# Kernel tuning notes

Measured on AMD Instinct MI355X. Metric: run time of the kernel, lower is better.

Reference implementation:

```python
import jax, jax.numpy as jnp
import numpy as np
from jax import lax

NEG = -1e30


def ctc_loss(log_probs, targets, input_lengths, target_lengths, blank=0):
    """CTC loss per sample (reduction='none').
    log_probs: [B,T,C] log-softmaxed. targets: [B,S] int (values != blank).
    Returns [B] negative log likelihoods.
    """
    B, T, C = log_probs.shape
    S = targets.shape[1]
    L = 2 * S + 1
    # extended label sequence with blanks interleaved: [b, t1, b, t2, ..., b]
    blanks = jnp.full((B, S), blank, targets.dtype)
    ext = jnp.concatenate(
        [jnp.stack([blanks, targets], axis=-1).reshape(B, 2 * S),
         jnp.full((B, 1), blank, targets.dtype)], axis=1)  # [B,L]
    # skip-transition allowed where ext[l] != blank and ext[l] != ext[l-2]
    prev2 = jnp.concatenate([jnp.full((B, 2), -1, ext.dtype), ext[:, :-2]], axis=1)
    allow_skip = (ext != blank) & (ext != prev2)  # [B,L]

    lp0 = jnp.take_along_axis(log_probs[:, 0, :], ext, axis=1)  # [B,L]
    alpha0 = jnp.where(jnp.arange(L)[None, :] < 2, lp0, NEG)

    def step(alpha, lp_t):  # lp_t: [B,C]
        lp = jnp.take_along_axis(lp_t, ext, axis=1)  # [B,L]
        a1 = alpha
        a2 = jnp.concatenate([jnp.full((B, 1), NEG), alpha[:, :-1]], axis=1)
        a3 = jnp.where(allow_skip,
                       jnp.concatenate([jnp.full((B, 2), NEG), alpha[:, :-2]], axis=1),
                       NEG)
        new = jax.nn.logsumexp(jnp.stack([a1, a2, a3]), axis=0) + lp
        return new, new

    _, alphas = lax.scan(step, alpha0, jnp.swapaxes(log_probs, 0, 1)[1:])
    alphas = jnp.concatenate([alpha0[None], alphas], axis=0)  # [T,B,L]

    t_idx = jnp.clip(input_lengths - 1, 0, T - 1)
    alpha_T = alphas[t_idx, jnp.arange(B)]  # [B,L]
    l1 = jnp.clip(2 * target_lengths, 0, L - 1)
    l2 = jnp.clip(2 * target_lengths - 1, 0, L - 1)
    last = jnp.take_along_axis(alpha_T, jnp.stack([l1, l2], axis=1), axis=1)  # [B,2]
    return -jax.nn.logsumexp(last, axis=1)


def focal_ctc(logits, targets, input_lengths, target_lengths, alpha=1.0, gamma=2.0):
    log_probs = jax.nn.log_softmax(logits, axis=-1)
    l = jnp.clip(ctc_loss(log_probs, targets, input_lengths, target_lengths), 1e-6, None)
    p_t = jnp.clip(jnp.exp(-l), 1e-6, 1.0)
    return jnp.mean(alpha * (1.0 - p_t) ** gamma * l)


def setup_inputs() -> dict:
    key = jax.random.key(0)
    ks = jax.random.split(key, 8)
    B, T = 32, 2000
    C_err, C_ph = 8, 128
    S_err, S_ph = 50, 200
    return {
        "error_logits": jax.random.normal(ks[0], (B, T, C_err), jnp.float32),
        "phoneme_logits": jax.random.normal(ks[1], (B, T, C_ph), jnp.float32),
        "error_targets": jax.random.randint(ks[2], (B, S_err), 1, C_err, jnp.int32),
        "phoneme_targets": jax.random.randint(ks[3], (B, S_ph), 1, C_ph, jnp.int32),
        "error_input_lengths": jnp.full((B,), T, jnp.int32),
        "phoneme_input_lengths": jnp.full((B,), T, jnp.int32),
        "error_target_lengths": jax.random.randint(ks[4], (B,), S_err // 2, S_err + 1, jnp.int32),
        "phoneme_target_lengths": jax.random.randint(ks[5], (B,), S_ph // 2, S_ph + 1, jnp.int32),
    }


def reference(error_logits, phoneme_logits, error_targets, phoneme_targets,
              error_input_lengths, phoneme_input_lengths,
              error_target_lengths, phoneme_target_lengths):
    error_weight, phoneme_weight = 1.0, 1.0
    err = focal_ctc(error_logits, error_targets, error_input_lengths, error_target_lengths)
    ph = focal_ctc(phoneme_logits, phoneme_targets, phoneme_input_lengths, phoneme_target_lengths)
    total = error_weight * err + phoneme_weight * ph
    return total, err, ph
```

## Files before the change

kernel.cpp:

```cpp
#include <hip/hip_runtime.h>
#include <hip/hip_bf16.h>

#define LOG2E 1.4426950408889634f
#define LN2   0.6931471805599453f
#define NEG2  (-1.4426950e30f)
#define EXP2F(x) __builtin_exp2f(x)
#define LOG2F(x) __builtin_log2f(x)
#define LDEXPF(x,k) __builtin_ldexpf((x),(k))

__device__ __forceinline__ float dpp_shr1_f(float x, float old) {
    return __int_as_float(__builtin_amdgcn_update_dpp(
        __float_as_int(old), __float_as_int(x), 0x138, 0xF, 0xF, false));
}
__device__ __forceinline__ int dpp_shr1_i(int x, int old) {
    return __builtin_amdgcn_update_dpp(old, x, 0x138, 0xF, 0xF, false);
}
__device__ __forceinline__ float dpp_shl1_f(float x, float old) {
    return __int_as_float(__builtin_amdgcn_update_dpp(
        __float_as_int(old), __float_as_int(x), 0x130, 0xF, 0xF, false));
}
__device__ __forceinline__ int dpp_shl1_i(int x, int old) {
    return __builtin_amdgcn_update_dpp(old, x, 0x130, 0xF, 0xF, false);
}

__device__ __forceinline__ unsigned bf16r(float x) {
    return (__float_as_uint(x) + 0x8000u) >> 16;
}

__device__ __forceinline__ void async16(void* lds, const void* g) {
    __builtin_amdgcn_global_load_lds(
        (const __attribute__((address_space(1))) unsigned int*)g,
        (__attribute__((address_space(3))) unsigned int*)lds, 16, 0, 0);
}
__device__ __forceinline__ void async4(void* lds, const void* g) {
    __builtin_amdgcn_global_load_lds(
        (const __attribute__((address_space(1))) unsigned int*)g,
        (__attribute__((address_space(3))) unsigned int*)lds, 4, 0, 0);
}

__device__ __forceinline__ void unpack8(const uint4& q, float (&p)[8]) {
    p[0] = __uint_as_float(q.x << 16);
    p[1] = __uint_as_float(q.x & 0xFFFF0000u);
    p[2] = __uint_as_float(q.y << 16);
    p[3] = __uint_as_float(q.y & 0xFFFF0000u);
    p[4] = __uint_as_float(q.z << 16);
    p[5] = __uint_as_float(q.z & 0xFFFF0000u);
    p[6] = __uint_as_float(q.w << 16);
    p[7] = __uint_as_float(q.w & 0xFFFF0000u);
}

__global__ __launch_bounds__(256) void ph_prob_kernel(
    const float* __restrict__ logits, const int* __restrict__ tgt,
    unsigned short* __restrict__ P) {
    int wid = threadIdx.x >> 6, lane = threadIdx.x & 63;
    int r = blockIdx.x * 4 + wid;
    int b = r / 2000;
    const float* row = logits + (size_t)r * 128;
    __shared__ float ylds[4][128];
    float y0 = row[lane] * LOG2E;
    float y1 = row[lane + 64] * LOG2E;
    ylds[wid][lane] = y0;
    ylds[wid][lane + 64] = y1;
    float m = fmaxf(y0, y1);
#pragma unroll
    for (int i = 1; i < 64; i <<= 1) m = fmaxf(m, __shfl_xor(m, i));
    float s = EXP2F(y0 - m) + EXP2F(y1 - m);
#pragma unroll
    for (int i = 1; i < 64; i <<= 1) s += __shfl_xor(s, i);
    float d2 = m + LOG2F(s);

    int c[4];
#pragma unroll
    for (int k = 0; k < 4; ++k) {
        int i = min(4 * lane + k, 199);
        c[k] = tgt[b * 200 + i];
    }
    float pb = EXP2F(ylds[wid][0] - d2);
    float po[4];
#pragma unroll
    for (int k = 0; k < 4; ++k) po[k] = EXP2F(ylds[wid][c[k]] - d2);

    unsigned h[8];
#pragma unroll
    for (int s2 = 0; s2 < 8; ++s2) {
        int l = 8 * lane + s2;
        float v = (s2 & 1) ? po[s2 >> 1] : pb;
        h[s2] = (l <= 400) ? bf16r(v) : 0u;
    }
    uint4 u;
    u.x = h[0] | (h[1] << 16);
    u.y = h[2] | (h[3] << 16);
    u.z = h[4] | (h[5] << 16);
    u.w = h[6] | (h[7] << 16);
    *(uint4*)(P + (size_t)r * 512 + lane * 8) = u;
}

__global__ __launch_bounds__(256) void err_prob_kernel(
    const float* __restrict__ logits, const int* __restrict__ tgt,
    unsigned short* __restrict__ P) {
    int wid = threadIdx.x >> 6, lane = threadIdx.x & 63;
    int r = blockIdx.x * 4 + wid;
    int b = r / 2000;
    const float* row = logits + (size_t)r * 8;
    __shared__ float ylds[4][8];
    float y = (lane < 8) ? row[lane] * LOG2E : -3.0e38f;
    if (lane < 8) ylds[wid][lane] = y;
    float m = y;
#pragma unroll
    for (int i = 1; i < 64; i <<= 1) m = fmaxf(m, __shfl_xor(m, i));
    float s = EXP2F(y - m);
#pragma unroll
    for (int i = 1; i < 64; i <<= 1) s += __shfl_xor(s, i);
    float d2 = m + LOG2F(s);

    int cc = tgt[b * 50 + min(lane, 49)];
    float pb = EXP2F(ylds[wid][0] - d2);
    float pod = EXP2F(ylds[wid][cc] - d2);
    int l0 = 2 * lane;
    unsigned h0 = (l0 <= 100) ? bf16r(pb) : 0u;
    unsigned h1 = (l0 + 1 <= 100) ? bf16r(pod) : 0u;
    *(unsigned*)(P + (size_t)r * 128 + lane * 2) = h0 | (h1 << 16);
}

__device__ __forceinline__ void finish_loss(float capA, float capB, int capEA,
                                            int capEB, int lane,
                                            float* __restrict__ loss_out, int b) {
    float vA = (capA > 0.f) ? (float)capEA + LOG2F(capA) : NEG2;
    float vB = (capB > 0.f) ? (float)capEB + LOG2F(capB) : NEG2;
    float mm = fmaxf(vA, vB);
#pragma unroll
    for (int i = 1; i < 64; i <<= 1) mm = fmaxf(mm, __shfl_xor(mm, i));
    float sum = EXP2F(vA - mm) + EXP2F(vB - mm);
#pragma unroll
    for (int i = 1; i < 64; i <<= 1) sum += __shfl_xor(sum, i);
    if (lane == 0) loss_out[b] = -(mm + LOG2F(sum)) * LN2;
}

__global__ __launch_bounds__(64) void ctc6_kernel(
    const unsigned short* __restrict__ Perr, const unsigned short* __restrict__ Pph,
    const int* __restrict__ err_tgt, const int* __restrict__ ph_tgt,
    const int* __restrict__ err_il, const int* __restrict__ ph_il,
    const int* __restrict__ err_tl, const int* __restrict__ ph_tl,
    float* __restrict__ aerr, int* __restrict__ aerrE,
    float* __restrict__ gerr, int* __restrict__ gerrE,
    float* __restrict__ aph, int* __restrict__ aphE,
    float* __restrict__ gph, int* __restrict__ gphE,
    float* __restrict__ loss_err, float* __restrict__ loss_ph, int T) {
    __shared__ unsigned short ring[32 * 512];
    char* ringc = (char*)ring;
    const int blk = blockIdx.x;
    const int lane = threadIdx.x & 63;
    const int NR = T >> 1;
    const int NCH = NR >> 3;

    if (blk < 32) {
        const int b = blk;
        int t_idx = min(max(err_il[b] - 1, 0), T - 1);
        const int* tgt = err_tgt + b * 50;
        float skip1f;
        {
            int l = lane * 2 + 1; bool sk = false;
            if (l >= 3 && l <= 100) { int i = l >> 1; sk = (tgt[i] != tgt[i - 1]); }
            skip1f = sk ? 1.f : 0.f;
        }
        const char* base = (const char*)(Perr + (size_t)b * T * 128);
        float a0 = 0.f, a1 = 0.f; int E = 0;

        auto fstep = [&](unsigned cur, bool rn) {
            float p0 = __uint_as_float(cur << 16);
            float p1 = __uint_as_float(cur & 0xFFFF0000u);
            float n1 = dpp_shr1_f(a1, 0.f);
            int En = dpp_shr1_i(E, E);
            int Ep = max(E, En);
            float t1 = LDEXPF(n1, En - Ep);
            float o0 = LDEXPF(a0, E - Ep), o1 = LDEXPF(a1, E - Ep);
            E = Ep;
            a0 = (o0 + t1) * p0;
            a1 = __builtin_fmaf(skip1f, t1, o1 + o0) * p1;
            if (rn) {
                float m = fmaxf(a0, a1);
                int k = ((__float_as_int(m) >> 23) & 255) - 127;
                a0 = LDEXPF(a0, -k); a1 = LDEXPF(a1, -k); E += k;
            }
        };

        if (t_idx == T - 1) {
            const char* srcl = base + lane * 4;
            auto rd = [&](int row) -> unsigned {
                return *((const unsigned*)(ringc + (size_t)(row & 31) * 256) + lane);
            };
#pragma unroll
            for (int r = 0; r < 24; ++r)
                async4(ringc + (size_t)(r & 31) * 256, srcl + (size_t)r * 256);
            {
#pragma unroll
                for (int r = 24; r < 32; ++r)
                    async4(ringc + (size_t)(r & 31) * 256, srcl + (size_t)r * 256);
                asm volatile("s_waitcnt vmcnt(16)" ::: "memory");
                __builtin_amdgcn_sched_barrier(0);
                unsigned q[8];
#pragma unroll
                for (int j = 0; j < 8; ++j) q[j] = rd(j);
                float p0 = __uint_as_float(q[0] << 16);
                float p1 = __uint_as_float(q[0] & 0xFFFF0000u);
                a0 = (lane == 0) ? p0 : 0.f;
                a1 = (lane == 0) ? p1 : 0.f;
                E = 0;
#pragma unroll
                for (int j = 1; j < 8; ++j) fstep(q[j], (j == 3) || (j == 7));
            }
            for (int k = 1; k < NCH; ++k) {
                if (k + 3 < NCH) {
                    int bs = (k + 3) * 8;
#pragma unroll
                    for (int r = 0; r < 8; ++r)
                        async4(ringc + (size_t)((bs + r) & 31) * 256,
                               srcl + (size_t)(bs + r) * 256);
                    asm volatile("s_waitcnt vmcnt(16)" ::: "memory");
                } else {
                    asm volatile("s_waitcnt vmcnt(0)" ::: "memory");
                }
                __builtin_amdgcn_sched_barrier(0);
                unsigned q[8];
#pragma unroll
                for (int j = 0; j < 8; ++j) q[j] = rd(k * 8 + j);
#pragma unroll
                for (int j = 0; j < 8; ++j) fstep(q[j], (j == 3) || (j == 7));
            }
            aerr[b * 128 + lane * 2] = a0;
            aerr[b * 128 + lane * 2 + 1] = a1;
            aerrE[b * 64 + lane] = E;
        } else {
            const int L = 101; int tl = err_tl[b];
            int l1 = min(2 * tl, L - 1), l2 = max(min(2 * tl - 1, L - 1), 0);
            float capA = 0.f, capB = 0.f; int capEA = 0, capEB = 0;
            for (int t = 0; t < T; ++t) {
                unsigned cur = *((const unsigned*)(base + (size_t)t * 256) + lane);
                if (t == 0) {
                    float p0 = __uint_as_float(cur << 16);
                    float p1 = __uint_as_float(cur & 0xFFFF0000u);
                    a0 = (lane == 0) ? p0 : 0.f;
                    a1 = (lane == 0) ? p1 : 0.f;
                    E = 0;
                } else {
                    fstep(cur, false);
                }
                if (t == t_idx) {
                    int l0 = lane * 2;
                    if (l0 == l1) { capA = a0; capEA = E; }
                    if (l0 == l2) { capB = a0; capEB = E; }
                    if (l0 + 1 == l1) { capA = a1; capEA = E; }
                    if (l0 + 1 == l2) { capB = a1; capEB = E; }
                }
                if ((t & 3) == 3) {
                    float m = fmaxf(a0, a1);
                    int k = ((__float_as_int(m) >> 23) & 255) - 127;
                    a0 = LDEXPF(a0, -k); a1 = LDEXPF(a1, -k); E += k;
                }
            }
            finish_loss(capA, capB, capEA, capEB, lane, loss_err, b);
        }

    } else if (blk < 64) {
        const int b = blk - 32;
        const int* tgt = err_tgt + b * 50;
        const int L = 101; int tl = err_tl[b];
        int l1 = min(2 * tl, L - 1), l2 = max(min(2 * tl - 1, L - 1), 0);
        float skip1f;
        {
            int l = lane * 2 + 1; bool sk = false;
            if (l >= 3 && l <= 100) { int i = l >> 1; sk = (tgt[i] != tgt[i - 1]); }
            skip1f = sk ? 1.f : 0.f;
        }
        float skp2 = dpp_shl1_f(skip1f, 0.f);
        const char* base = (const char*)(Perr + (size_t)b * T * 128);
        const char* srcl = base + (size_t)(T - 1) * 256 + lane * 4;
        auto rd = [&](int row) -> unsigned {
            return *((const unsigned*)(ringc + (size_t)(row & 31) * 256) + lane);
        };
        float g0 = 0.f, g1 = 0.f; int E = 0;
        auto bstep = [&](unsigned cur, bool rn) {
            float p0 = __uint_as_float(cur << 16);
            float p1 = __uint_as_float(cur & 0xFFFF0000u);
            float nb0 = dpp_shl1_f(g0, 0.f), nb1 = dpp_shl1_f(g1, 0.f);
            int En = dpp_shl1_i(E, E);
            int Ep = max(E, En);
            float o0 = LDEXPF(g0, E - Ep), o1 = LDEXPF(g1, E - Ep);
            float t0 = LDEXPF(nb0, En - Ep), t1 = LDEXPF(nb1, En - Ep);
            E = Ep;
            g0 = (o0 + o1) * p0;
            g1 = __builtin_fmaf(skp2, t1, o1 + t0) * p1;
            if (rn) {
                float m = fmaxf(g0, g1);
                int k = ((__float_as_int(m) >> 23) & 255) - 127;
                g0 = LDEXPF(g0, -k); g1 = LDEXPF(g1, -k); E += k;
            }
        };
#pragma unroll
        for (int r = 0; r < 24; ++r)
            async4(ringc + (size_t)(r & 31) * 256, srcl - (size_t)r * 256);
        {
#pragma unroll
            for (int r = 24; r < 32; ++r)
                async4(ringc + (size_t)(r & 31) * 256, srcl - (size_t)r * 256);
            asm volatile("s_waitcnt vmcnt(16)" ::: "memory");
            __builtin_amdgcn_sched_barrier(0);
            unsigned q[8];
#pragma unroll
            for (int j = 0; j < 8; ++j) q[j] = rd(j);
            float p0 = __uint_as_float(q[0] << 16);
            float p1 = __uint_as_float(q[0] & 0xFFFF0000u);
            int l0 = lane * 2;
            g0 = (l0 == l1 || l0 == l2) ? p0 : 0.f;
            g1 = (l0 + 1 == l1 || l0 + 1 == l2) ? p1 : 0.f;
            E = 0;
#pragma unroll
            for (int j = 1; j < 8; ++j) bstep(q[j], (j == 3) || (j == 7));
        }
        for (int k = 1; k < NCH; ++k) {
            if (k + 3 < NCH) {
                int bs = (k + 3) * 8;
#pragma unroll
                for (int r = 0; r < 8; ++r)
                    async4(ringc + (size_t)((bs + r) & 31) * 256,
                           srcl - (size_t)(bs + r) * 256);
                asm volatile("s_waitcnt vmcnt(16)" ::: "memory");
            } else {
                asm volatile("s_waitcnt vmcnt(0)" ::: "memory");
            }
            __builtin_amdgcn_sched_barrier(0);
            unsigned q[8];
#pragma unroll
            for (int j = 0; j < 8; ++j) q[j] = rd(k * 8 + j);
#pragma unroll
            for (int j = 0; j < 8; ++j) bstep(q[j], (j == 3) || (j == 7));
        }
        gerr[b * 128 + lane * 2] = g0;
        gerr[b * 128 + lane * 2 + 1] = g1;
        gerrE[b * 64 + lane] = E;

    } else if (blk < 96) {
        const int b = blk - 64;
        int t_idx = min(max(ph_il[b] - 1, 0), T - 1);
        const int* tgt = ph_tgt + b * 200;
        float skf[8];
#pragma unroll
        for (int s = 0; s < 8; ++s) {
            int l = lane * 8 + s; float v = 0.f;
            if ((s & 1) && l >= 3 && l <= 400) {
                int i = l >> 1; v = (tgt[i] != tgt[i - 1]) ? 1.f : 0.f;
            }
            skf[s] = v;
        }
        const char* base = (const char*)(Pph + (size_t)b * T * 512);
        float a[8];
#pragma unroll
        for (int s = 0; s < 8; ++s) a[s] = 0.f;
        int E = 0;
        auto rd4 = [&](int row) -> uint4 {
            return *((const uint4*)(ringc + (size_t)(row & 31) * 1024) + lane);
        };
        auto fstep = [&](const uint4& q, bool rn) {
            float p[8]; unpack8(q, p);
            float n7 = dpp_shr1_f(a[7], 0.f), n6 = dpp_shr1_f(a[6], 0.f);
            int En = dpp_shr1_i(E, E);
            int Ep = max(E, En);
            float o[8];
#pragma unroll
            for (int s = 0; s < 8; ++s) o[s] = LDEXPF(a[s], E - Ep);
            float s7 = LDEXPF(n7, En - Ep), s6 = LDEXPF(n6, En - Ep);
            E = Ep;
#pragma unroll
            for (int s = 0; s < 8; ++s) {
                float am1 = (s == 0) ? s7 : o[s - 1];
                float am2 = (s == 0) ? s6 : ((s == 1) ? s7 : o[s - 2]);
                a[s] = __builtin_fmaf(skf[s], am2, o[s] + am1) * p[s];
            }
            if (rn) {
                float m = a[0];
#pragma unroll
                for (int s = 1; s < 8; ++s) m = fmaxf(m, a[s]);
                int k = ((__float_as_int(m) >> 23) & 255) - 127;
#pragma unroll
                for (int s = 0; s < 8; ++s) a[s] = LDEXPF(a[s], -k);
                E += k;
            }
        };

        if (t_idx == T - 1) {
            const char* srcl = base + lane * 16;
#pragma unroll
            for (int r = 0; r < 24; ++r)
                async16(ringc + (size_t)(r & 31) * 1024, srcl + (size_t)r * 1024);
            {
#pragma unroll
                for (int r = 24; r < 32; ++r)
                    async16(ringc + (size_t)(r & 31) * 1024, srcl + (size_t)r * 1024);
                asm volatile("s_waitcnt vmcnt(16)" ::: "memory");
                __builtin_amdgcn_sched_barrier(0);
                uint4 q[8];
#pragma unroll
                for (int j = 0; j < 8; ++j) q[j] = rd4(j);
                float p[8]; unpack8(q[0], p);
#pragma unroll
                for (int s = 0; s < 8; ++s) {
                    int l = lane * 8 + s;
                    a[s] = (l < 2) ? p[s] : 0.f;
                }
                E = 0;
#pragma unroll
                for (int j = 1; j < 8; ++j) fstep(q[j], (j == 3) || (j == 7));
            }
            for (int k = 1; k < NCH; ++k) {
                if (k + 3 < NCH) {
                    int bs = (k + 3) * 8;
#pragma unroll
                    for (int r = 0; r < 8; ++r)
                        async16(ringc + (size_t)((bs + r) & 31) * 1024,
                                srcl + (size_t)(bs + r) * 1024);
                    asm volatile("s_waitcnt vmcnt(16)" ::: "memory");
                } else {
                    asm volatile("s_waitcnt vmcnt(0)" ::: "memory");
                }
                __builtin_amdgcn_sched_barrier(0);
                uint4 q[8];
#pragma unroll
                for (int j = 0; j < 8; ++j) q[j] = rd4(k * 8 + j);
#pragma unroll
                for (int j = 0; j < 8; ++j) fstep(q[j], (j == 3) || (j == 7));
            }
#pragma unroll
            for (int s = 0; s < 8; ++s) aph[b * 512 + lane * 8 + s] = a[s];
            aphE[b * 64 + lane] = E;
        } else {
            const int L = 401; int tl = ph_tl[b];
            int l1 = min(2 * tl, L - 1), l2 = max(min(2 * tl - 1, L - 1), 0);
            float capA = 0.f, capB = 0.f; int capEA = 0, capEB = 0;
            for (int t = 0; t < T; ++t) {
                uint4 q = *((const uint4*)(base + (size_t)t * 1024) + lane);
                if (t == 0) {
                    float p[8]; unpack8(q, p);
#pragma unroll
                    for (int s = 0; s < 8; ++s) {
                        int l = lane * 8 + s;
                        a[s] = (l < 2) ? p[s] : 0.f;
                    }
                    E = 0;
                } else {
                    fstep(q, false);
                }
                if (t == t_idx) {
#pragma unroll
                    for (int s = 0; s < 8; ++s) {
                        int l = lane * 8 + s;
                        if (l == l1) { capA = a[s]; capEA = E; }
                        if (l == l2) { capB = a[s]; capEB = E; }
                    }
                }
                if ((t & 3) == 3) {
                    float m = a[0];
#pragma unroll
                    for (int s = 1; s < 8; ++s) m = fmaxf(m, a[s]);
                    int k = ((__float_as_int(m) >> 23) & 255) - 127;
#pragma unroll
                    for (int s = 0; s < 8; ++s) a[s] = LDEXPF(a[s], -k);
                    E += k;
                }
            }
            finish_loss(capA, capB, capEA, capEB, lane, loss_ph, b);
        }

    } else {
        const int b = blk - 96;
        const int* tgt = ph_tgt + b * 200;
        const int L = 401; int tl = ph_tl[b];
        int l1 = min(2 * tl, L - 1), l2 = max(min(2 * tl - 1, L - 1), 0);
        float skf[8];
#pragma unroll
        for (int s = 0; s < 8; ++s) {
            int l = lane * 8 + s; float v = 0.f;
            if ((s & 1) && l >= 3 && l <= 400) {
                int i = l >> 1; v = (tgt[i] != tgt[i - 1]) ? 1.f : 0.f;
            }
            skf[s] = v;
        }
        float nskf1 = dpp_shl1_f(skf[1], 0.f);
        float skp2[8];
        skp2[0] = 0.f; skp2[1] = skf[3]; skp2[2] = 0.f; skp2[3] = skf[5];
        skp2[4] = 0.f; skp2[5] = skf[7]; skp2[6] = 0.f; skp2[7] = nskf1;

        const char* base = (const char*)(Pph + (size_t)b * T * 512);
        const char* srcl = base + (size_t)(T - 1) * 1024 + lane * 16;
        auto rd4 = [&](int row) -> uint4 {
            return *((const uint4*)(ringc + (size_t)(row & 31) * 1024) + lane);
        };
        float g[8];
#pragma unroll
        for (int s = 0; s < 8; ++s) g[s] = 0.f;
        int E = 0;
        auto bstep = [&](const uint4& q, bool rn) {
            float p[8]; unpack8(q, p);
            float nb0 = dpp_shl1_f(g[0], 0.f), nb1 = dpp_shl1_f(g[1], 0.f);
            int En = dpp_shl1_i(E, E);
            int Ep = max(E, En);
            float o[8];
#pragma unroll
            for (int s = 0; s < 8; ++s) o[s] = LDEXPF(g[s], E - Ep);
            float t0 = LDEXPF(nb0, En - Ep), t1 = LDEXPF(nb1, En - Ep);
            E = Ep;
#pragma unroll
            for (int s = 0; s < 8; ++s) {
                float bp1 = (s < 7) ? o[s + 1] : t0;
                float bp2 = (s < 6) ? o[s + 2] : ((s == 6) ? t0 : t1);
                g[s] = __builtin_fmaf(skp2[s], bp2, o[s] + bp1) * p[s];
            }
            if (rn) {
                float m = g[0];
#pragma unroll
                for (int s = 1; s < 8; ++s) m = fmaxf(m, g[s]);
                int k = ((__float_as_int(m) >> 23) & 255) - 127;
#pragma unroll
                for (int s = 0; s < 8; ++s) g[s] = LDEXPF(g[s], -k);
                E += k;
            }
        };
#pragma unroll
        for (int r = 0; r < 24; ++r)
            async16(ringc + (size_t)(r & 31) * 1024, srcl - (size_t)r * 1024);
        {
#pragma unroll
            for (int r = 24; r < 32; ++r)
                async16(ringc + (size_t)(r & 31) * 1024, srcl - (size_t)r * 1024);
            asm volatile("s_waitcnt vmcnt(16)" ::: "memory");
            __builtin_amdgcn_sched_barrier(0);
            uint4 q[8];
#pragma unroll
            for (int j = 0; j < 8; ++j) q[j] = rd4(j);
            float p[8]; unpack8(q[0], p);
#pragma unroll
            for (int s = 0; s < 8; ++s) {
                int l = lane * 8 + s;
                g[s] = (l == l1 || l == l2) ? p[s] : 0.f;
            }
            E = 0;
#pragma unroll
            for (int j = 1; j < 8; ++j) bstep(q[j], (j == 3) || (j == 7));
        }
        for (int k = 1; k < NCH; ++k) {
            if (k + 3 < NCH) {
                int bs = (k + 3) * 8;
#pragma unroll
                for (int r = 0; r < 8; ++r)
                    async16(ringc + (size_t)((bs + r) & 31) * 1024,
                            srcl - (size_t)(bs + r) * 1024);
                asm volatile("s_waitcnt vmcnt(16)" ::: "memory");
            } else {
                asm volatile("s_waitcnt vmcnt(0)" ::: "memory");
            }
            __builtin_amdgcn_sched_barrier(0);
            uint4 q[8];
#pragma unroll
            for (int j = 0; j < 8; ++j) q[j] = rd4(k * 8 + j);
#pragma unroll
            for (int j = 0; j < 8; ++j) bstep(q[j], (j == 3) || (j == 7));
        }
#pragma unroll
        for (int s = 0; s < 8; ++s) gph[b * 512 + lane * 8 + s] = g[s];
        gphE[b * 64 + lane] = E;
    }
}

__global__ __launch_bounds__(64) void combine_kernel(
    const int* __restrict__ err_tgt, const int* __restrict__ ph_tgt,
    const int* __restrict__ err_il, const int* __restrict__ ph_il,
    const float* __restrict__ aerr, const int* __restrict__ aerrE,
    const float* __restrict__ gerr, const int* __restrict__ gerrE,
    const float* __restrict__ aph, const int* __restrict__ aphE,
    const float* __restrict__ gph, const int* __restrict__ gphE,
    float* __restrict__ loss_err, float* __restrict__ loss_ph, int T) {
    const int blk = blockIdx.x;
    const int lane = threadIdx.x & 63;
    if (blk < 32) {
        const int b = blk;
        int t_idx = min(max(err_il[b] - 1, 0), T - 1);
        if (t_idx != T - 1) return;
        const int* tgt = err_tgt + b * 50;
        float skip1f;
        {
            int l = lane * 2 + 1; bool sk = false;
            if (l >= 3 && l <= 100) { int i = l >> 1; sk = (tgt[i] != tgt[i - 1]); }
            skip1f = sk ? 1.f : 0.f;
        }
        float a0 = aerr[b * 128 + lane * 2], a1 = aerr[b * 128 + lane * 2 + 1];
        int Ea = aerrE[b * 64 + lane];
        float g0 = gerr[b * 128 + lane * 2], g1 = gerr[b * 128 + lane * 2 + 1];
        int Eb = gerrE[b * 64 + lane];
        float nb0 = __shfl_down(g0, 1), nb1 = __shfl_down(g1, 1);
        int Ebn = __shfl_down(Eb, 1);
        float skp2 = __shfl_down(skip1f, 1);
        if (lane == 63) { nb0 = 0.f; nb1 = 0.f; Ebn = Eb; skp2 = 0.f; }
        int Em = max(Eb, Ebn);
        float o0 = LDEXPF(g0, Eb - Em), o1 = LDEXPF(g1, Eb - Em);
        float t0 = LDEXPF(nb0, Ebn - Em), t1 = LDEXPF(nb1, Ebn - Em);
        float bc0 = o0 + o1;
        float bc1 = __builtin_fmaf(skp2, t1, o1 + t0);
        float dot = __builtin_fmaf(a0, bc0, a1 * bc1);
        float v = (dot > 0.f) ? (float)(Ea + Em) + LOG2F(dot) : NEG2;
        float mm = v;
#pragma unroll
        for (int i = 1; i < 64; i <<= 1) mm = fmaxf(mm, __shfl_xor(mm, i));
        float sum = EXP2F(v - mm);
#pragma unroll
        for (int i = 1; i < 64; i <<= 1) sum += __shfl_xor(sum, i);
        if (lane == 0) loss_err[b] = -(mm + LOG2F(sum)) * LN2;
    } else {
        const int b = blk - 32;
        int t_idx = min(max(ph_il[b] - 1, 0), T - 1);
        if (t_idx != T - 1) return;
        const int* tgt = ph_tgt + b * 200;
        float skf[8];
#pragma unroll
        for (int s = 0; s < 8; ++s) {
            int l = lane * 8 + s; float v = 0.f;
            if ((s & 1) && l >= 3 && l <= 400) {
                int i = l >> 1; v = (tgt[i] != tgt[i - 1]) ? 1.f : 0.f;
            }
            skf[s] = v;
        }
        float a[8], g[8];
#pragma unroll
        for (int s = 0; s < 8; ++s) {
            a[s] = aph[b * 512 + lane * 8 + s];
            g[s] = gph[b * 512 + lane * 8 + s];
        }
        int Ea = aphE[b * 64 + lane];
        int Eb = gphE[b * 64 + lane];
        float nb0 = __shfl_down(g[0], 1), nb1 = __shfl_down(g[1], 1);
        int Ebn = __shfl_down(Eb, 1);
        float nskf1 = __shfl_down(skf[1], 1);
        if (lane == 63) { nb0 = 0.f; nb1 = 0.f; Ebn = Eb; nskf1 = 0.f; }
        float skp2[8];
        skp2[0] = 0.f; skp2[1] = skf[3]; skp2[2] = 0.f; skp2[3] = skf[5];
        skp2[4] = 0.f; skp2[5] = skf[7]; skp2[6] = 0.f; skp2[7] = nskf1;
        int Em = max(Eb, Ebn);
        float o[8];
#pragma unroll
        for (int s = 0; s < 8; ++s) o[s] = LDEXPF(g[s], Eb - Em);
        float t0 = LDEXPF(nb0, Ebn - Em), t1 = LDEXPF(nb1, Ebn - Em);
        float dot = 0.f;
#pragma unroll
        for (int s = 0; s < 8; ++s) {
            float bp1 = (s < 7) ? o[s + 1] : t0;
            float bp2 = (s < 6) ? o[s + 2] : ((s == 6) ? t0 : t1);
            float bc = __builtin_fmaf(skp2[s], bp2, o[s] + bp1);
            dot = __builtin_fmaf(a[s], bc, dot);
        }
        float v = (dot > 0.f) ? (float)(Ea + Em) + LOG2F(dot) : NEG2;
        float mm = v;
#pragma unroll
        for (int i = 1; i < 64; i <<= 1) mm = fmaxf(mm, __shfl_xor(mm, i));
        float sum = EXP2F(v - mm);
#pragma unroll
        for (int i = 1; i < 64; i <<= 1) sum += __shfl_xor(sum, i);
        if (lane == 0) loss_ph[b] = -(mm + LOG2F(sum)) * LN2;
    }
}

__global__ void denom_err_kernel(const float* __restrict__ logits,
                                 float* __restrict__ d2, int rows) {
    int r = blockIdx.x * blockDim.x + threadIdx.x;
    if (r >= rows) return;
    const float* row = logits + (size_t)r * 8;
    float x[8];
#pragma unroll
    for (int i = 0; i < 8; ++i) x[i] = row[i] * LOG2E;
    float m = x[0];
#pragma unroll
    for (int i = 1; i < 8; ++i) m = fmaxf(m, x[i]);
    float s = 0.f;
#pragma unroll
    for (int i = 0; i < 8; ++i) s += EXP2F(x[i] - m);
    d2[r] = m + LOG2F(s);
}

__global__ void denom_ph_kernel(const float* __restrict__ logits,
                                float* __restrict__ d2, int rows) {
    int wave = (int)((blockIdx.x * (size_t)blockDim.x + threadIdx.x) >> 6);
    int lane = threadIdx.x & 63;
    if (wave >= rows) return;
    const float* row = logits + (size_t)wave * 128;
    float x0 = row[lane] * LOG2E;
    float x1 = row[lane + 64] * LOG2E;
    float m = fmaxf(x0, x1);
#pragma unroll
    for (int i = 1; i < 64; i <<= 1) m = fmaxf(m, __shfl_xor(m, i));
    float s = EXP2F(x0 - m) + EXP2F(x1 - m);
#pragma unroll
    for (int i = 1; i < 64; i <<= 1) s += __shfl_xor(s, i);
    if (lane == 0) d2[wave] = m + LOG2F(s);
}

template <int NST, int C>
__device__ __forceinline__ void gather_row(const float* ringL, const float* ringD,
                                           int row, const int (&clsoff)[NST],
                                           float (&g)[NST], float& gd) {
    int base = (row & 63) * C;
#pragma unroll
    for (int s = 0; s < NST; ++s) g[s] = ringL[base + clsoff[s]];
    gd = ringD[row & 63];
}

template <int C, int CHV>
__device__ __forceinline__ void stage_load(const float* __restrict__ lrow,
                                           const float* __restrict__ d2row,
                                           int t0, int T, int lane,
                                           float4 (&st)[CHV], float4& stD) {
#pragma unroll
// ... 93 lines not shown
        int li = v ? l : 0;
        int c = 0;
        bool sk = false;
        if (li & 1) {
            int i = li >> 1;
            c = tgt[i];
            if (li >= 3) sk = (c != tgt[i - 1]);
        }
        clsoff[s] = c;
        skipb[s] = sk;
        validf[s] = v ? 1.f : 0.f;
    }
    float4 st[CHV];
    float4 stD = make_float4(0.f, 0.f, 0.f, 0.f);
    stage_load<C, CHV>(lrow, d2row, 0, T, lane, st, stD);
    stage_write<C, CHV>(ringL, ringD, 0, lane, st, stD);
    stage_load<C, CHV>(lrow, d2row, 32, T, lane, st, stD);
    stage_write<C, CHV>(ringL, ringD, 32, lane, st, stD);
    stage_load<C, CHV>(lrow, d2row, 64, T, lane, st, stD);
    float gA[NST], gB[NST], dA, dB;
    gather_row<NST, C>(ringL, ringD, 0, clsoff, gA, dA);
    gather_row<NST, C>(ringL, ringD, 1, clsoff, gB, dB);
    float a[NST];
#pragma unroll
    for (int s = 0; s < NST; ++s) a[s] = 0.f;
    int E = 0;
    float capA = 0.f, capB = 0.f;
    int capEA = 0, capEB = 0;
    const int NCH = (T + 31) >> 5;
    for (int c = 0; c < NCH; ++c) {
        int t0 = c << 5;
        int half = min(32, T - t0) >> 1;
        for (int j = 0; j < half; ++j) {
            int t = t0 + 2 * j;
            do_step_lin<NST>(a, E, gA, dA, validf, skipb, lane, t, t_idx, l1, l2,
                             capA, capB, capEA, capEB);
            gather_row<NST, C>(ringL, ringD, t + 2, clsoff, gA, dA);
            do_step_lin<NST>(a, E, gB, dB, validf, skipb, lane, t + 1, t_idx, l1, l2,
                             capA, capB, capEA, capEB);
            gather_row<NST, C>(ringL, ringD, t + 3, clsoff, gB, dB);
            if (j == 14 && c + 2 < NCH) {
                stage_write<C, CHV>(ringL, ringD, t0 + 64, lane, st, stD);
                if (c + 3 < NCH)
                    stage_load<C, CHV>(lrow, d2row, t0 + 96, T, lane, st, stD);
            }
        }
    }
    float vA = (capA > 0.f) ? (float)capEA + LOG2F(capA) : NEG2;
    float vB = (capB > 0.f) ? (float)capEB + LOG2F(capB) : NEG2;
    float mm = fmaxf(vA, vB);
#pragma unroll
    for (int i = 1; i < 64; i <<= 1) mm = fmaxf(mm, __shfl_xor(mm, i));
    float sum = EXP2F(vA - mm) + EXP2F(vB - mm);
#pragma unroll
    for (int i = 1; i < 64; i <<= 1) sum += __shfl_xor(sum, i);
    if (lane == 0) loss_out[b] = -(mm + LOG2F(sum)) * LN2;
}

__global__ __launch_bounds__(64) void ctc_kernel(
    const float* __restrict__ err_logits, const float* __restrict__ ph_logits,
    const int* __restrict__ err_tgt, const int* __restrict__ ph_tgt,
    const int* __restrict__ err_il, const int* __restrict__ ph_il,
    const int* __restrict__ err_tl, const int* __restrict__ ph_tl,
    const float* __restrict__ d2_err, const float* __restrict__ d2_ph,
    float* __restrict__ loss_err, float* __restrict__ loss_ph, int T) {
    __shared__ float ringL[64 * 128];
    __shared__ float ringD[64];
    int blk = blockIdx.x;
    if (blk < 32) {
        int b = blk;
        const int L = 101;
        int tl = err_tl[b];
        int l1 = min(2 * tl, L - 1);
        int l2 = max(min(2 * tl - 1, L - 1), 0);
        int t_idx = min(max(err_il[b] - 1, 0), T - 1);
        ctc_run<2, 8, 50, 1>(err_logits + (size_t)b * T * 8, d2_err + (size_t)b * T,
                             err_tgt + b * 50, T, t_idx, l1, l2, ringL, ringD,
                             loss_err, b);
    } else {
        int b = blk - 32;
        const int L = 401;
        int tl = ph_tl[b];
        int l1 = min(2 * tl, L - 1);
        int l2 = max(min(2 * tl - 1, L - 1), 0);
        int t_idx = min(max(ph_il[b] - 1, 0), T - 1);
        ctc_run<8, 128, 200, 16>(ph_logits + (size_t)b * T * 128, d2_ph + (size_t)b * T,
                                 ph_tgt + b * 200, T, t_idx, l1, l2, ringL, ringD,
                                 loss_ph, b);
    }
}

__global__ void final_kernel(const float* __restrict__ loss_err,
                             const float* __restrict__ loss_ph,
                             float* __restrict__ out) {
    int lane = threadIdx.x & 63;
    float fe = 0.f, fp = 0.f;
    if (lane < 32) {
        float l = fmaxf(loss_err[lane], 1e-6f);
        float pt = fminf(fmaxf(EXP2F(-l * LOG2E), 1e-6f), 1.0f);
        float om = 1.f - pt;
        fe = om * om * l;
        l = fmaxf(loss_ph[lane], 1e-6f);
        pt = fminf(fmaxf(EXP2F(-l * LOG2E), 1e-6f), 1.0f);
        om = 1.f - pt;
        fp = om * om * l;
    }
#pragma unroll
    for (int i = 1; i < 64; i <<= 1) {
        fe += __shfl_xor(fe, i);
        fp += __shfl_xor(fp, i);
    }
    if (lane == 0) {
        float err = fe / 32.f;
        float ph = fp / 32.f;
        out[0] = err + ph;
        out[1] = err;
        out[2] = ph;
    }
}

extern "C" void kernel_launch(void* const* d_in, const int* in_sizes, int n_in,
                              void* d_out, int out_size, void* d_ws, size_t ws_size,
                              hipStream_t stream) {
    const int B = 32, T = 2000;
    const float* err_logits = (const float*)d_in[0];
    const float* ph_logits  = (const float*)d_in[1];
    const int* err_tgt = (const int*)d_in[2];
    const int* ph_tgt  = (const int*)d_in[3];
    const int* err_il  = (const int*)d_in[4];
    const int* ph_il   = (const int*)d_in[5];
    const int* err_tl  = (const int*)d_in[6];
    const int* ph_tl   = (const int*)d_in[7];
    float* out = (float*)d_out;

    const size_t PH_US  = (size_t)B * T * 512;
    const size_t ERR_US = (size_t)B * T * 128;

    char* p = (char*)d_ws;
    unsigned short* Pph  = (unsigned short*)p; p += PH_US * 2;
    unsigned short* Perr = (unsigned short*)p; p += ERR_US * 2;
    float* aph  = (float*)p; p += (size_t)B * 512 * 4;
    int*   aphE = (int*)p;   p += (size_t)B * 64 * 4;
    float* gph  = (float*)p; p += (size_t)B * 512 * 4;
    int*   gphE = (int*)p;   p += (size_t)B * 64 * 4;
    float* aerr = (float*)p; p += (size_t)B * 128 * 4;
    int*   aerrE= (int*)p;   p += (size_t)B * 64 * 4;
    float* gerr = (float*)p; p += (size_t)B * 128 * 4;
    int*   gerrE= (int*)p;   p += (size_t)B * 64 * 4;
    float* loss_err = (float*)p; p += B * 4;
    float* loss_ph  = (float*)p; p += B * 4;
    const size_t need = (size_t)(p - (char*)d_ws);

    if (ws_size >= need) {
        ph_prob_kernel<<<(B * T) / 4, 256, 0, stream>>>(ph_logits, ph_tgt, Pph);
        err_prob_kernel<<<(B * T) / 4, 256, 0, stream>>>(err_logits, err_tgt, Perr);
        ctc6_kernel<<<128, 64, 0, stream>>>(Perr, Pph, err_tgt, ph_tgt,
                                            err_il, ph_il, err_tl, ph_tl,
                                            aerr, aerrE, gerr, gerrE,
                                            aph, aphE, gph, gphE,
                                            loss_err, loss_ph, T);
        combine_kernel<<<64, 64, 0, stream>>>(err_tgt, ph_tgt, err_il, ph_il,
                                              aerr, aerrE, gerr, gerrE,
                                              aph, aphE, gph, gphE,
                                              loss_err, loss_ph, T);
        final_kernel<<<1, 64, 0, stream>>>(loss_err, loss_ph, out);
    } else {
        float* ws = (float*)d_ws;
        float* d2_err   = ws;
        float* d2_ph    = ws + 64000;
        float* le = ws + 128000;
        float* lp = ws + 128032;
        int rows = B * T;
        denom_err_kernel<<<(rows + 255) / 256, 256, 0, stream>>>(err_logits, d2_err, rows);
        denom_ph_kernel<<<rows / 4, 256, 0, stream>>>(ph_logits, d2_ph, rows);
        ctc_kernel<<<64, 64, 0, stream>>>(err_logits, ph_logits, err_tgt, ph_tgt,
                                          err_il, ph_il, err_tl, ph_tl,
                                          d2_err, d2_ph, le, lp, T);
        final_kernel<<<1, 64, 0, stream>>>(le, lp, out);
    }
}
```

Before: 184.4 us.

## Fuse prob kernels and hoist neighbor exponent alignment out of per-step recursion

Merges the phoneme and error probability kernels into one launch, with the grid split by block index. In the CTC forward and backward recursions, the per-timestep exponent alignment between neighbouring lanes (a DPP shift of E plus several ldexp calls) is moved into the periodic renormalization. A cached power-of-two scale factor f is applied to the shifted neighbour values at each step instead. This shortens the serial per-timestep dependency chain, at the cost of the neighbour's relative scale going stale for up to four steps. The d>=-127 clamp and the four-step growth between renormalizations could affect precision in edge cases.

```diff
diff --git a/kernel.cpp b/kernel.cpp
--- a/kernel.cpp
+++ b/kernel.cpp
@@ -49,77 +49,75 @@
     p[7] = __uint_as_float(q.w & 0xFFFF0000u);
 }
 
-__global__ __launch_bounds__(256) void ph_prob_kernel(
-    const float* __restrict__ logits, const int* __restrict__ tgt,
-    unsigned short* __restrict__ P) {
+__global__ __launch_bounds__(256) void prob_kernel(
+    const float* __restrict__ ph_logits, const int* __restrict__ ph_tgt,
+    unsigned short* __restrict__ Pph,
+    const float* __restrict__ err_logits, const int* __restrict__ err_tgt,
+    unsigned short* __restrict__ Perr) {
     int wid = threadIdx.x >> 6, lane = threadIdx.x & 63;
-    int r = blockIdx.x * 4 + wid;
-    int b = r / 2000;
-    const float* row = logits + (size_t)r * 128;
     __shared__ float ylds[4][128];
-    float y0 = row[lane] * LOG2E;
-    float y1 = row[lane + 64] * LOG2E;
-    ylds[wid][lane] = y0;
-    ylds[wid][lane + 64] = y1;
-    float m = fmaxf(y0, y1);
-#pragma unroll
-    for (int i = 1; i < 64; i <<= 1) m = fmaxf(m, __shfl_xor(m, i));
-    float s = EXP2F(y0 - m) + EXP2F(y1 - m);
-#pragma unroll
-    for (int i = 1; i < 64; i <<= 1) s += __shfl_xor(s, i);
-    float d2 = m + LOG2F(s);
-
-    int c[4];
-#pragma unroll
-    for (int k = 0; k < 4; ++k) {
-        int i = min(4 * lane + k, 199);
-        c[k] = tgt[b * 200 + i];
-    }
-    float pb = EXP2F(ylds[wid][0] - d2);
-    float po[4];
-#pragma unroll
-    for (int k = 0; k < 4; ++k) po[k] = EXP2F(ylds[wid][c[k]] - d2);
-
-    unsigned h[8];
-#pragma unroll
-    for (int s2 = 0; s2 < 8; ++s2) {
-        int l = 8 * lane + s2;
-        float v = (s2 & 1) ? po[s2 >> 1] : pb;
-        h[s2] = (l <= 400) ? bf16r(v) : 0u;
-    }
-    uint4 u;
-    u.x = h[0] | (h[1] << 16);
-    u.y = h[2] | (h[3] << 16);
-    u.z = h[4] | (h[5] << 16);
-    u.w = h[6] | (h[7] << 16);
-    *(uint4*)(P + (size_t)r * 512 + lane * 8) = u;
-}
-
-__global__ __launch_bounds__(256) void err_prob_kernel(
-    const float* __restrict__ logits, const int* __restrict__ tgt,
-    unsigned short* __restrict__ P) {
-    int wid = threadIdx.x >> 6, lane = threadIdx.x & 63;
-    int r = blockIdx.x * 4 + wid;
-    int b = r / 2000;
-    const float* row = logits + (size_t)r * 8;
-    __shared__ float ylds[4][8];
-    float y = (lane < 8) ? row[lane] * LOG2E : -3.0e38f;
-    if (lane < 8) ylds[wid][lane] = y;
-    float m = y;
-#pragma unroll
-    for (int i = 1; i < 64; i <<= 1) m = fmaxf(m, __shfl_xor(m, i));
-    float s = EXP2F(y - m);
-#pragma unroll
-    for (int i = 1; i < 64; i <<= 1) s += __shfl_xor(s, i);
-    float d2 = m + LOG2F(s);
-
-    int cc = tgt[b * 50 + min(lane, 49)];
-    float pb = EXP2F(ylds[wid][0] - d2);
-    float pod = EXP2F(ylds[wid][cc] - d2);
-    int l0 = 2 * lane;
-    unsigned h0 = (l0 <= 100) ? bf16r(pb) : 0u;
-    unsigned h1 = (l0 + 1 <= 100) ? bf16r(pod) : 0u;
-    *(unsigned*)(P + (size_t)r * 128 + lane * 2) = h0 | (h1 << 16);
+    if (blockIdx.x < 16000) {
+        int r = blockIdx.x * 4 + wid;
+        int b = r / 2000;
+        const float* row = ph_logits + (size_t)r * 128;
+        float y0 = row[lane] * LOG2E;
+        float y1 = row[lane + 64] * LOG2E;
+        ylds[wid][lane] = y0;
+        ylds[wid][lane + 64] = y1;
+        float m = fmaxf(y0, y1);
+#pragma unroll
+        for (int i = 1; i < 64; i <<= 1) m = fmaxf(m, __shfl_xor(m, i));
+        float s = EXP2F(y0 - m) + EXP2F(y1 - m);
+#pragma unroll
+        for (int i = 1; i < 64; i <<= 1) s += __shfl_xor(s, i);
+        float d2 = m + LOG2F(s);
+
+        int c[4];
+#pragma unroll
+        for (int k = 0; k < 4; ++k) {
+            int i = min(4 * lane + k, 199);
+            c[k] = ph_tgt[b * 200 + i];
+        }
+        float pb = EXP2F(ylds[wid][0] - d2);
+        float po[4];
+#pragma unroll
+        for (int k = 0; k < 4; ++k) po[k] = EXP2F(ylds[wid][c[k]] - d2);
+
+        unsigned h[8];
+#pragma unroll
+        for (int s2 = 0; s2 < 8; ++s2) {
+            int l = 8 * lane + s2;
+            float v = (s2 & 1) ? po[s2 >> 1] : pb;
+            h[s2] = (l <= 400) ? bf16r(v) : 0u;
+        }
+        uint4 u;
+        u.x = h[0] | (h[1] << 16);
+        u.y = h[2] | (h[3] << 16);
+        u.z = h[4] | (h[5] << 16);
+        u.w = h[6] | (h[7] << 16);
+        *(uint4*)(Pph + (size_t)r * 512 + lane * 8) = u;
+    } else {
+        int r = (blockIdx.x - 16000) * 4 + wid;
+        int b = r / 2000;
+        const float* row = err_logits + (size_t)r * 8;
+        float y = (lane < 8) ? row[lane] * LOG2E : -3.0e38f;
+        if (lane < 8) ylds[wid][lane] = y;
+        float m = y;
+#pragma unroll
+        for (int i = 1; i < 64; i <<= 1) m = fmaxf(m, __shfl_xor(m, i));
+        float s = EXP2F(y - m);
+#pragma unroll
+        for (int i = 1; i < 64; i <<= 1) s += __shfl_xor(s, i);
+        float d2 = m + LOG2F(s);
+
+        int cc = err_tgt[b * 50 + min(lane, 49)];
+        float pb = EXP2F(ylds[wid][0] - d2);
+        float pod = EXP2F(ylds[wid][cc] - d2);
+        int l0 = 2 * lane;
+        unsigned h0 = (l0 <= 100) ? bf16r(pb) : 0u;
+        unsigned h1 = (l0 + 1 <= 100) ? bf16r(pod) : 0u;
+        *(unsigned*)(Perr + (size_t)r * 128 + lane * 2) = h0 | (h1 << 16);
+    }
 }
 
 __device__ __forceinline__ void finish_loss(float capA, float capB, int capEA,
@@ -136,7 +134,7 @@
     if (lane == 0) loss_out[b] = -(mm + LOG2F(sum)) * LN2;
 }
 
-__global__ __launch_bounds__(64) void ctc6_kernel(
+__global__ __launch_bounds__(64) void ctc7_kernel(
     const unsigned short* __restrict__ Perr, const unsigned short* __restrict__ Pph,
     const int* __restrict__ err_tgt, const int* __restrict__ ph_tgt,
     const int* __restrict__ err_il, const int* __restrict__ ph_il,
@@ -164,24 +162,27 @@
             skip1f = sk ? 1.f : 0.f;
         }
         const char* base = (const char*)(Perr + (size_t)b * T * 128);
-        float a0 = 0.f, a1 = 0.f; int E = 0;
-
-        auto fstep = [&](unsigned cur, bool rn) {
+        float a0 = 0.f, a1 = 0.f; int E = 0; float f = 1.f;
+
+        auto fstep = [&](unsigned cur) {
             float p0 = __uint_as_float(cur << 16);
             float p1 = __uint_as_float(cur & 0xFFFF0000u);
-            float n1 = dpp_shr1_f(a1, 0.f);
+            float t1 = dpp_shr1_f(a1, 0.f) * f;
+            float na0 = (a0 + t1) * p0;
+            a1 = __builtin_fmaf(skip1f, t1, a1 + a0) * p1;
+            a0 = na0;
+        };
+        auto rex = [&]() {
+            float m = fmaxf(a0, a1);
+            int k = ((__float_as_int(m) >> 23) & 255) - 127;
+            a0 = LDEXPF(a0, -k); a1 = LDEXPF(a1, -k); E += k;
             int En = dpp_shr1_i(E, E);
             int Ep = max(E, En);
-            float t1 = LDEXPF(n1, En - Ep);
-            float o0 = LDEXPF(a0, E - Ep), o1 = LDEXPF(a1, E - Ep);
+            int eo = E - Ep;
+            a0 = LDEXPF(a0, eo); a1 = LDEXPF(a1, eo);
             E = Ep;
-            a0 = (o0 + t1) * p0;
-            a1 = __builtin_fmaf(skip1f, t1, o1 + o0) * p1;
-            if (rn) {
-                float m = fmaxf(a0, a1);
-                int k = ((__float_as_int(m) >> 23) & 255) - 127;
-                a0 = LDEXPF(a0, -k); a1 = LDEXPF(a1, -k); E += k;
-            }
+            int d = max(En - Ep, -127);
+            f = __int_as_float((d + 127) << 23);
         };
 
         if (t_idx == T - 1) {
@@ -205,9 +206,12 @@
                 float p1 = __uint_as_float(q[0] & 0xFFFF0000u);
                 a0 = (lane == 0) ? p0 : 0.f;
                 a1 = (lane == 0) ? p1 : 0.f;
-                E = 0;
-#pragma unroll
-                for (int j = 1; j < 8; ++j) fstep(q[j], (j == 3) || (j == 7));
+                E = 0; f = 1.f;
+#pragma unroll
+                for (int j = 1; j < 8; ++j) {
+                    fstep(q[j]);
+                    if (j == 3 || j == 7) rex();
+                }
             }
             for (int k = 1; k < NCH; ++k) {
                 if (k + 3 < NCH) {
@@ -225,7 +229,10 @@
 #pragma unroll
                 for (int j = 0; j < 8; ++j) q[j] = rd(k * 8 + j);
 #pragma unroll
-                for (int j = 0; j < 8; ++j) fstep(q[j], (j == 3) || (j == 7));
+                for (int j = 0; j < 8; ++j) {
+                    fstep(q[j]);
+                    if (j == 3 || j == 7) rex();
+                }
             }
             aerr[b * 128 + lane * 2] = a0;
             aerr[b * 128 + lane * 2 + 1] = a1;
@@ -236,14 +243,21 @@
             float capA = 0.f, capB = 0.f; int capEA = 0, capEB = 0;
             for (int t = 0; t < T; ++t) {
                 unsigned cur = *((const unsigned*)(base + (size_t)t * 256) + lane);
+                float p0 = __uint_as_float(cur << 16);
+                float p1 = __uint_as_float(cur & 0xFFFF0000u);
                 if (t == 0) {
-                    float p0 = __uint_as_float(cur << 16);
-                    float p1 = __uint_as_float(cur & 0xFFFF0000u);
                     a0 = (lane == 0) ? p0 : 0.f;
                     a1 = (lane == 0) ? p1 : 0.f;
                     E = 0;
                 } else {
-                    fstep(cur, false);
+                    float n1 = dpp_shr1_f(a1, 0.f);
+                    int En = dpp_shr1_i(E, E);
+                    int Ep = max(E, En);
+                    float t1 = LDEXPF(n1, En - Ep);
+                    float o0 = LDEXPF(a0, E - Ep), o1 = LDEXPF(a1, E - Ep);
+                    E = Ep;
+                    a0 = (o0 + t1) * p0;
+                    a1 = __builtin_fmaf(skip1f, t1, o1 + o0) * p1;
                 }
                 if (t == t_idx) {
                     int l0 = lane * 2;
@@ -278,23 +292,27 @@
         auto rd = [&](int row) -> unsigned {
             return *((const unsigned*)(ringc + (size_t)(row & 31) * 256) + lane);
         };
-        float g0 = 0.f, g1 = 0.f; int E = 0;
-        auto bstep = [&](unsigned cur, bool rn) {
+        float g0 = 0.f, g1 = 0.f; int E = 0; float f = 1.f;
+        auto bstep = [&](unsigned cur) {
             float p0 = __uint_as_float(cur << 16);
             float p1 = __uint_as_float(cur & 0xFFFF0000u);
-            float nb0 = dpp_shl1_f(g0, 0.f), nb1 = dpp_shl1_f(g1, 0.f);
+            float t0 = dpp_shl1_f(g0, 0.f) * f;
+            float t1 = dpp_shl1_f(g1, 0.f) * f;
+            float ng0 = (g0 + g1) * p0;
+            g1 = __builtin_fmaf(skp2, t1, g1 + t0) * p1;
+            g0 = ng0;
+        };
+        auto rex = [&]() {
+            float m = fmaxf(g0, g1);
+            int k = ((__float_as_int(m) >> 23) & 255) - 127;
+            g0 = LDEXPF(g0, -k); g1 = LDEXPF(g1, -k); E += k;
             int En = dpp_shl1_i(E, E);
             int Ep = max(E, En);
-            float o0 = LDEXPF(g0, E - Ep), o1 = LDEXPF(g1, E - Ep);
-            float t0 = LDEXPF(nb0, En - Ep), t1 = LDEXPF(nb1, En - Ep);
+            int eo = E - Ep;
+            g0 = LDEXPF(g0, eo); g1 = LDEXPF(g1, eo);
             E = Ep;
-            g0 = (o0 + o1) * p0;
-            g1 = __builtin_fmaf(skp2, t1, o1 + t0) * p1;
-            if (rn) {
-                float m = fmaxf(g0, g1);
-                int k = ((__float_as_int(m) >> 23) & 255) - 127;
-                g0 = LDEXPF(g0, -k); g1 = LDEXPF(g1, -k); E += k;
-            }
+            int d = max(En - Ep, -127);
+            f = __int_as_float((d + 127) << 23);
         };
 #pragma unroll
         for (int r = 0; r < 24; ++r)
@@ -313,9 +331,12 @@
             int l0 = lane * 2;
             g0 = (l0 == l1 || l0 == l2) ? p0 : 0.f;
             g1 = (l0 + 1 == l1 || l0 + 1 == l2) ? p1 : 0.f;
-            E = 0;
-#pragma unroll
-            for (int j = 1; j < 8; ++j) bstep(q[j], (j == 3) || (j == 7));
+            E = 0; f = 1.f;
+#pragma unroll
+            for (int j = 1; j < 8; ++j) {
+                bstep(q[j]);
+                if (j == 3 || j == 7) rex();
+            }
         }
         for (int k = 1; k < NCH; ++k) {
             if (k + 3 < NCH) {
@@ -333,7 +354,10 @@
 #pragma unroll
             for (int j = 0; j < 8; ++j) q[j] = rd(k * 8 + j);
 #pragma unroll
-            for (int j = 0; j < 8; ++j) bstep(q[j], (j == 3) || (j == 7));
+            for (int j = 0; j < 8; ++j) {
+                bstep(q[j]);
+                if (j == 3 || j == 7) rex();
+            }
         }
         gerr[b * 128 + lane * 2] = g0;
         gerr[b * 128 + lane * 2 + 1] = g1;
@@ -356,35 +380,40 @@
         float a[8];
 #pragma unroll
         for (int s = 0; s < 8; ++s) a[s] = 0.f;
-        int E = 0;
+        int E = 0; float f = 1.f;
         auto rd4 = [&](int row) -> uint4 {
             return *((const uint4*)(ringc + (size_t)(row & 31) * 1024) + lane);
         };
-        auto fstep = [&](const uint4& q, bool rn) {
+        auto fstep = [&](const uint4& q) {
             float p[8]; unpack8(q, p);
-            float n7 = dpp_shr1_f(a[7], 0.f), n6 = dpp_shr1_f(a[6], 0.f);
+            float n7 = dpp_shr1_f(a[7], 0.f) * f;
+            float n6 = dpp_shr1_f(a[6], 0.f) * f;
+            float an[8];
+#pragma unroll
+            for (int s = 0; s < 8; ++s) {
+                float am1 = (s == 0) ? n7 : a[s - 1];
+                float am2 = (s == 0) ? n6 : ((s == 1) ? n7 : a[s - 2]);
+                an[s] = __builtin_fmaf(skf[s], am2, a[s] + am1) * p[s];
+            }
+#pragma unroll
+            for (int s = 0; s < 8; ++s) a[s] = an[s];
+        };
+        auto rex = [&]() {
+            float m = a[0];
+#pragma unroll
+            for (int s = 1; s < 8; ++s) m = fmaxf(m, a[s]);
+            int k = ((__float_as_int(m) >> 23) & 255) - 127;
+#pragma unroll
+            for (int s = 0; s < 8; ++s) a[s] = LDEXPF(a[s], -k);
+            E += k;
             int En = dpp_shr1_i(E, E);
             int Ep = max(E, En);
-            float o[8];
-#pragma unroll
-            for (int s = 0; s < 8; ++s) o[s] = LDEXPF(a[s], E - Ep);
-            float s7 = LDEXPF(n7, En - Ep), s6 = LDEXPF(n6, En - Ep);
+            int eo = E - Ep;
+#pragma unroll
+            for (int s = 0; s < 8; ++s) a[s] = LDEXPF(a[s], eo);
             E = Ep;
-#pragma unroll
-            for (int s = 0; s < 8; ++s) {
-                float am1 = (s == 0) ? s7 : o[s - 1];
-                float am2 = (s == 0) ? s6 : ((s == 1) ? s7 : o[s - 2]);
-                a[s] = __builtin_fmaf(skf[s], am2, o[s] + am1) * p[s];
-            }
-            if (rn) {
-                float m = a[0];
-#pragma unroll
-                for (int s = 1; s < 8; ++s) m = fmaxf(m, a[s]);
-                int k = ((__float_as_int(m) >> 23) & 255) - 127;
-#pragma unroll
-                for (int s = 0; s < 8; ++s) a[s] = LDEXPF(a[s], -k);
-                E += k;
-            }
+            int d = max(En - Ep, -127);
+            f = __int_as_float((d + 127) << 23);
         };
 
         if (t_idx == T - 1) {
@@ -407,9 +436,12 @@
                     int l = lane * 8 + s;
                     a[s] = (l < 2) ? p[s] : 0.f;
                 }
-                E = 0;
-#pragma unroll
-                for (int j = 1; j < 8; ++j) fstep(q[j], (j == 3) || (j == 7));
+                E = 0; f = 1.f;
+#pragma unroll
+                for (int j = 1; j < 8; ++j) {
+                    fstep(q[j]);
+                    if (j == 3 || j == 7) rex();
+                }
             }
             for (int k = 1; k < NCH; ++k) {
                 if (k + 3 < NCH) {
@@ -427,7 +459,10 @@
 #pragma unroll
                 for (int j = 0; j < 8; ++j) q[j] = rd4(k * 8 + j);
 #pragma unroll
-                for (int j = 0; j < 8; ++j) fstep(q[j], (j == 3) || (j == 7));
+                for (int j = 0; j < 8; ++j) {
+                    fstep(q[j]);
+                    if (j == 3 || j == 7) rex();
+                }
             }
 #pragma unroll
             for (int s = 0; s < 8; ++s) aph[b * 512 + lane * 8 + s] = a[s];
@@ -438,8 +473,8 @@
             float capA = 0.f, capB = 0.f; int capEA = 0, capEB = 0;
             for (int t = 0; t < T; ++t) {
                 uint4 q = *((const uint4*)(base + (size_t)t * 1024) + lane);
+                float p[8]; unpack8(q, p);
                 if (t == 0) {
-                    float p[8]; unpack8(q, p);
 #pragma unroll
                     for (int s = 0; s < 8; ++s) {
                         int l = lane * 8 + s;
@@ -447,7 +482,20 @@
                     }
                     E = 0;
                 } else {
-                    fstep(q, false);
+                    float n7 = dpp_shr1_f(a[7], 0.f), n6 = dpp_shr1_f(a[6], 0.f);
+                    int En = dpp_shr1_i(E, E);
+                    int Ep = max(E, En);
+                    float o[8];
+#pragma unroll
+                    for (int s = 0; s < 8; ++s) o[s] = LDEXPF(a[s], E - Ep);
+                    float s7 = LDEXPF(n7, En - Ep), s6 = LDEXPF(n6, En - Ep);
+                    E = Ep;
+#pragma unroll
+                    for (int s = 0; s < 8; ++s) {
+                        float am1 = (s == 0) ? s7 : o[s - 1];
+                        float am2 = (s == 0) ? s6 : ((s == 1) ? s7 : o[s - 2]);
+                        a[s] = __builtin_fmaf(skf[s], am2, o[s] + am1) * p[s];
+                    }
                 }
                 if (t == t_idx) {
 #pragma unroll
@@ -497,32 +545,37 @@
         float g[8];
 #pragma unroll
         for (int s = 0; s < 8; ++s) g[s] = 0.f;
-        int E = 0;
-        auto bstep = [&](const uint4& q, bool rn) {
+        int E = 0; float f = 1.f;
+        auto bstep = [&](const uint4& q) {
             float p[8]; unpack8(q, p);
-            float nb0 = dpp_shl1_f(g[0], 0.f), nb1 = dpp_shl1_f(g[1], 0.f);
+            float nb0 = dpp_shl1_f(g[0], 0.f) * f;
+            float nb1 = dpp_shl1_f(g[1], 0.f) * f;
+            float gn[8];
+#pragma unroll
+            for (int s = 0; s < 8; ++s) {
+                float bp1 = (s < 7) ? g[s + 1] : nb0;
+                float bp2 = (s < 6) ? g[s + 2] : ((s == 6) ? nb0 : nb1);
+                gn[s] = __builtin_fmaf(skp2[s], bp2, g[s] + bp1) * p[s];
+            }
+#pragma unroll
+            for (int s = 0; s < 8; ++s) g[s] = gn[s];
+        };
+        auto rex = [&]() {
+            float m = g[0];
+#pragma unroll
+            for (int s = 1; s < 8; ++s) m = fmaxf(m, g[s]);
+            int k = ((__float_as_int(m) >> 23) & 255) - 127;
+#pragma unroll
+            for (int s = 0; s < 8; ++s) g[s] = LDEXPF(g[s], -k);
+            E += k;
             int En = dpp_shl1_i(E, E);
             int Ep = max(E, En);
-            float o[8];
-#pragma unroll
-            for (int s = 0; s < 8; ++s) o[s] = LDEXPF(g[s], E - Ep);
-            float t0 = LDEXPF(nb0, En - Ep), t1 = LDEXPF(nb1, En - Ep);
+            int eo = E - Ep;
+#pragma unroll
+            for (int s = 0; s < 8; ++s) g[s] = LDEXPF(g[s], eo);
             E = Ep;
-#pragma unroll
-            for (int s = 0; s < 8; ++s) {
-                float bp1 = (s < 7) ? o[s + 1] : t0;
-                float bp2 = (s < 6) ? o[s + 2] : ((s == 6) ? t0 : t1);
-                g[s] = __builtin_fmaf(skp2[s], bp2, o[s] + bp1) * p[s];
-            }
-            if (rn) {
-                float m = g[0];
-#pragma unroll
-                for (int s = 1; s < 8; ++s) m = fmaxf(m, g[s]);
-                int k = ((__float_as_int(m) >> 23) & 255) - 127;
-#pragma unroll
-                for (int s = 0; s < 8; ++s) g[s] = LDEXPF(g[s], -k);
-                E += k;
-            }
+            int d = max(En - Ep, -127);
+            f = __int_as_float((d + 127) << 23);
         };
 #pragma unroll
         for (int r = 0; r < 24; ++r)
@@ -542,9 +595,12 @@
                 int l = lane * 8 + s;
                 g[s] = (l == l1 || l == l2) ? p[s] : 0.f;
             }
-            E = 0;
-#pragma unroll
-            for (int j = 1; j < 8; ++j) bstep(q[j], (j == 3) || (j == 7));
+            E = 0; f = 1.f;
+#pragma unroll
+            for (int j = 1; j < 8; ++j) {
+                bstep(q[j]);
+                if (j == 3 || j == 7) rex();
+            }
         }
         for (int k = 1; k < NCH; ++k) {
             if (k + 3 < NCH) {
@@ -562,7 +618,10 @@
 #pragma unroll
             for (int j = 0; j < 8; ++j) q[j] = rd4(k * 8 + j);
 #pragma unroll
-            for (int j = 0; j < 8; ++j) bstep(q[j], (j == 3) || (j == 7));
+            for (int j = 0; j < 8; ++j) {
+                bstep(q[j]);
+                if (j == 3 || j == 7) rex();
+            }
         }
 #pragma unroll
         for (int s = 0; s < 8; ++s) gph[b * 512 + lane * 8 + s] = g[s];
@@ -962,9 +1021,9 @@
     const size_t need = (size_t)(p - (char*)d_ws);
 
     if (ws_size >= need) {
-        ph_prob_kernel<<<(B * T) / 4, 256, 0, stream>>>(ph_logits, ph_tgt, Pph);
-        err_prob_kernel<<<(B * T) / 4, 256, 0, stream>>>(err_logits, err_tgt, Perr);
-        ctc6_kernel<<<128, 64, 0, stream>>>(Perr, Pph, err_tgt, ph_tgt,
+        prob_kernel<<<32000, 256, 0, stream>>>(ph_logits, ph_tgt, Pph,
+                                               err_logits, err_tgt, Perr);
+        ctc7_kernel<<<128, 64, 0, stream>>>(Perr, Pph, err_tgt, ph_tgt,
                                             err_il, ph_il, err_tl, ph_tl,
                                             aerr, aerrE, gerr, gerrE,
                                             aph, aphE, gph, gphE,
```

New measurement: 167.8 us. 1.1x faster.
